# Optimization experiments

Hardware: AMD Instinct MI355X
Metric: run time of the kernel (lower is better)

## Reference

```python
import jax
import jax.numpy as jnp
import numpy as np

N_WIRES = 4          # hardcoded by QLayer encoder (rx on wires 0..3)
H = N_WIRES          # hidden_dim must equal n_qubits for the gating elementwise math
T, B, D, TAGS = 512, 2048, 8, 16  # original unbinds dim 0, so dim0 = time, dim1 = batch


def apply_rx(state, theta, wire):
    """Apply RX(theta) on `wire`. state: (B,2,2,2,2) complex64, theta: (B,)."""
    st = jnp.moveaxis(state, 1 + wire, -1)
    a, b = st[..., 0], st[..., 1]
    th = theta[:, None, None, None] * 0.5
    c = jnp.cos(th)
    s = -1j * jnp.sin(th)
    st = jnp.stack([c * a + s * b, s * a + c * b], axis=-1)
    return jnp.moveaxis(st, -1, 1 + wire)


def apply_cnot(state, ctrl, tgt):
    st = jnp.moveaxis(state, (1 + ctrl, 1 + tgt), (-2, -1))  # (...,2,2)
    st = st.at[..., 1, :].set(st[..., 1, ::-1])
    return jnp.moveaxis(st, (-2, -1), (1 + ctrl, 1 + tgt))


def qlayer(angles, thetas):
    """QuantumQLSTM.QLayer: RX data encoding, trainable RX, CNOT ring, PauliZ expvals.
    angles: (B, 4) data angles; thetas: (4,) trainable RX angles -> (B, 4) expvals."""
    bsz = angles.shape[0]
    state = jnp.zeros((bsz, 16), jnp.complex64).at[:, 0].set(1.0)
    state = state.reshape(bsz, 2, 2, 2, 2)
    for w in range(N_WIRES):
        state = apply_rx(state, angles[:, w], w)
    for w in range(N_WIRES):
        state = apply_rx(state, jnp.broadcast_to(thetas[w], (bsz,)), w)
    for w in range(N_WIRES):  # cnot(w, w+1), last wraps to 0
        state = apply_cnot(state, w, (w + 1) % N_WIRES)
    probs = state.real ** 2 + state.imag ** 2  # (B,2,2,2,2)
    exps = []
    for w in range(N_WIRES):
        sign = jnp.array([1.0, -1.0], jnp.float32).reshape(
            [1] + [2 if i == w else 1 for i in range(N_WIRES)])
        exps.append(jnp.sum(probs * sign, axis=(1, 2, 3, 4)))
    return jnp.stack(exps, axis=-1)  # (B, 4)


def lstm_forward(x, w_gates, b_gates, rx_theta):
    # Faithful to torch: inputs.unbind(dim=0) -> scan over axis 0; batch = x.shape[1].
    bsz = x.shape[1]
    h0 = jnp.zeros((bsz, H), x.dtype)
    c0 = jnp.zeros((bsz, H), x.dtype)

    def step(carry, xt):
        hx, cx = carry
        comb = jnp.concatenate([xt, hx], axis=-1)                    # (B, D+H)
        pre = jnp.einsum('bd,gkd->gbk', comb, w_gates) + b_gates[:, None, :]  # (4,B,4)
        f = jax.nn.sigmoid(qlayer(pre[0], rx_theta[0]))
        i = jax.nn.sigmoid(qlayer(pre[1], rx_theta[1]))
        g = jnp.tanh(qlayer(pre[2], rx_theta[2]))
        o = jax.nn.sigmoid(qlayer(pre[3], rx_theta[3]))
        cx = f * cx + i * g
        hx = o * jnp.tanh(cx)
        return (hx, cx), hx

    _, outs = jax.lax.scan(jax.checkpoint(step), (h0, c0), x)
    return outs  # (T, B, H)


def setup_inputs() -> dict:
    key = jax.random.key(0)
    ks = jax.random.split(key, 6)
    x = jax.random.normal(ks[0], (T, B, D), jnp.float32)
    w_gates = jax.random.normal(ks[1], (4, N_WIRES, D + H), jnp.float32) * 0.3
    b_gates = jnp.zeros((4, N_WIRES), jnp.float32)
    rx_theta = jax.random.uniform(ks[2], (4, N_WIRES), jnp.float32, 0.0, 2.0 * np.pi)
    w_tag = jax.random.normal(ks[3], (TAGS, H), jnp.float32) * 0.3
    b_tag = jnp.zeros((TAGS,), jnp.float32)
    return {"x": x, "w_gates": w_gates, "b_gates": b_gates,
            "rx_theta": rx_theta, "w_tag": w_tag, "b_tag": b_tag}


def reference(x, w_gates, b_gates, rx_theta, w_tag, b_tag):
    # encode(): SamplerQNN has input_params=[], so it cannot transform features;
    # features pass through to the QLSTM (see notes).
    outs = lstm_forward(x, w_gates, b_gates, rx_theta)   # (T, B, H)
    logits = outs @ w_tag.T + b_tag                      # (T, B, TAGS)
    return jax.nn.log_softmax(logits, axis=-1)
```

## Files before the change

kernel.cpp:

```cpp
#include <hip/hip_runtime.h>

#define TT   512
#define BB   2048
#define NTAG 16
#define CH   8
#define NCH  (TT / CH)
#define BBN  (BB * NTAG)

typedef float v2f __attribute__((ext_vector_type(2)));

#define DPP_XOR1  0xB1
#define DPP_XOR2  0x4E
#define DPP_XOR3  0x1B
#define DPP_ROR4  0x124
#define DPP_ROR8  0x128
#define DPP_ROR12 0x12C
#define DPP_BC0   0x00
#define DPP_BC1   0x55
#define DPP_BC2   0xAA
#define DPP_BC3   0xFF

template<int CTRL>
__device__ __forceinline__ float dppf(float v) {
    int r = __builtin_amdgcn_update_dpp(0, __builtin_bit_cast(int, v),
                                        CTRL, 0xF, 0xF, true);
    return __builtin_bit_cast(float, r);
}

#define PINV(x) asm volatile("" : "+v"(x))

__global__ __launch_bounds__(256, 1) void qlstm_fused(
    const float* __restrict__ x,
    const float* __restrict__ w_gates,
    const float* __restrict__ b_gates,
    const float* __restrict__ rx_theta,
    const float* __restrict__ w_tag,
    const float* __restrict__ b_tag,
    float* __restrict__ out)
{
    __shared__ float  accL[2][4][CH][64];
    __shared__ float  hrng[2][2][CH][64];
    __shared__ float4 xstg[2][2][64];

    const int tid = threadIdx.x;
    const int wv  = tid >> 6;
    const int l   = tid & 63;
    const int e   = l >> 4;

    const float IV  = 0.15915494309189535f;
    const float L2E = 1.44269504088896f;
    const float LN2 = 0.69314718056f;

    if (wv < 2) {
        const int s = wv;
        const int w = (l >> 2) & 3;
        const int G = l & 3;

        const float* wrow = w_gates + (G * 4 + w) * 12;
        float wh0 = wrow[8 + ((w + 0) & 3)] * IV;
        float wh1 = wrow[8 + ((w + 1) & 3)] * IV;
        float wh2 = wrow[8 + ((w + 2) & 3)] * IV;
        float wh3 = wrow[8 + ((w + 3) & 3)] * IV;

        const bool gt = (G == 2);
        float ab = gt ? 0.0f : 0.5f;
        float d0 = gt ? 0.999904f  : 0.25f;
        float d1 = gt ? -0.331065f : -0.0208333333f;
        float d2 = gt ? 0.120472f  : 0.00208333333f;
        float d3 = gt ? -0.027717f : -2.10813e-4f;

        float u0 = 0.999160f,  u1 = -0.325289f, u2 = 0.112257f;
        float u3 = -0.028766f, u4 = 0.0043665f, u5 = -0.00028186f;

        const bool w0 = (w == 0), w1 = (w == 1), w3 = (w == 3);

        PINV(wh0); PINV(wh1); PINV(wh2); PINV(wh3);
        PINV(ab);  PINV(d0);  PINV(d1);  PINV(d2);  PINV(d3);
        PINV(u0);  PINV(u1);  PINV(u2);  PINV(u3);  PINV(u4);  PINV(u5);

        const int atl = (l & 48) | ((l & 3) << 2) | ((l >> 2) & 3);

        float h = 0.f, c = 0.f;

        __syncthreads();

        float a[CH];
        {
            const float* ap0 = &accL[s][0][0][atl];
            #pragma unroll
            for (int i = 0; i < CH; ++i) a[i] = ap0[i * 64];
        }

        for (int cc = 0; cc < NCH; ++cc) {
            const float* np = &accL[s][(cc + 1) & 3][0][atl];
            float n[CH];
            #pragma unroll
            for (int i = 0; i < CH; ++i) n[i] = np[i * 64];

            float* hp = &hrng[s][cc & 1][0][l];

            #pragma unroll
            for (int i = 0; i < CH; ++i) {
                const float s1 = fmaf(h, wh0, a[i]);
                const float s2 = fmaf(dppf<DPP_ROR12>(h), wh1, s1);
                const float mm = dppf<DPP_ROR8>(h) * wh2;
                const float s3 = fmaf(dppf<DPP_ROR4>(h), wh3, mm);
                const float ang = s2 + s3;

                const float C = __builtin_amdgcn_cosf(ang);

                const float n1 = dppf<DPP_ROR12>(C);
                const float n2 = dppf<DPP_ROR8>(C);
                const float n3 = dppf<DPP_ROR4>(C);
                const float Bp = n2 * n3;
                const float pp = C * n1;
                const float F1  = w0 ? n1 : C;
                const float F1b = w3 ? pp : F1;
                const float F2  = w1 ? n3 : Bp;
                const float q   = F1b * F2;

                const float y  = q * q;
                const float y2 = y * y;
                const float tA = fmaf(y, d1, d0);
                const float tB = fmaf(y, d3, d2);
                const float P  = fmaf(y2, tB, tA);
                const float act = fmaf(q, P, ab);

                const float A2  = dppf<DPP_BC2>(act);
                const float A12 = dppf<DPP_BC1>(act) * A2;
                c = fmaf(dppf<DPP_BC0>(act), c, A12);

                const float voc = dppf<DPP_BC3>(act) * c;
                const float cy  = c * c;
                const float cy2 = cy * cy;
                const float t1  = fmaf(cy, u1, u0);
                const float t2  = fmaf(cy, u3, u2);
                const float t3  = fmaf(cy, u5, u4);
                const float t4  = fmaf(cy2, t3, t2);
                const float m1v = voc * t1;
                const float vc2 = voc * cy2;
                const float hr  = fmaf(vc2, t4, m1v);

                hp[i * 64] = hr;
                h = hr;
            }

            #pragma unroll
            for (int i = 0; i < CH; ++i) a[i] = n[i];

            __syncthreads();
        }
    } else {
        const int s  = wv - 2;
        const int b0 = blockIdx.x * 8 + s * 4;
        const int g  = (l >> 2) & 3;
        const int k  = l & 3;

        const float* wrow = w_gates + (g * 4 + k) * 12;
        const v2f wp0 = { wrow[0] * IV, wrow[1] * IV };
        const v2f wp1 = { wrow[2] * IV, wrow[3] * IV };
        const v2f wp2 = { wrow[4] * IV, wrow[5] * IV };
        const v2f wp3 = { wrow[6] * IV, wrow[7] * IV };
        const v2f bp  = { (b_gates[g * 4 + k] + rx_theta[g * 4 + k]) * IV, 0.0f };

        const int tag = g * 4 + k;
        const float wt0 = w_tag[tag * 4 + (k ^ 0)] * L2E;
        const float wt1 = w_tag[tag * 4 + (k ^ 1)] * L2E;
        const float wt2 = w_tag[tag * 4 + (k ^ 2)] * L2E;
        const float wt3 = w_tag[tag * 4 + (k ^ 3)] * L2E;
        const float bt  = b_tag[tag] * L2E;

        const int hsl = e * 16 + k * 4;
        float* outp = out + (size_t)b0 * NTAG + l;

        const float* xlane = x + (size_t)(l >> 3) * (BB * 8)
                               + (size_t)b0 * 8 + (l & 7) * 4;
        const size_t CHOFF = (size_t)CH * BB * 8;

        auto compute_acc = [&](int xbuf, int ring) {
            float* ap = &accL[s][ring][0][l];
            #pragma unroll
            for (int i = 0; i < CH; ++i) {
                const float4 xA = xstg[s][xbuf][i * 8 + 2 * e];
                const float4 xB = xstg[s][xbuf][i * 8 + 2 * e + 1];
                const v2f a01 = { xA.x, xA.y }, a23 = { xA.z, xA.w };
                const v2f a45 = { xB.x, xB.y }, a67 = { xB.z, xB.w };
                v2f acc = __builtin_elementwise_fma(a01, wp0, bp);
                acc = __builtin_elementwise_fma(a23, wp1, acc);
                acc = __builtin_elementwise_fma(a45, wp2, acc);
                acc = __builtin_elementwise_fma(a67, wp3, acc);
                ap[i * 64] = acc.x + acc.y;
            }
        };

        float4 reg = *(const float4*)(xlane);
        xstg[s][0][l] = reg;
        reg = *(const float4*)(xlane + CHOFF);
        xstg[s][1][l] = reg;
        compute_acc(0, 0);
        compute_acc(1, 1);
        reg = *(const float4*)(xlane + 2 * CHOFF);
        xstg[s][0][l] = reg;
        reg = *(const float4*)(xlane + 3 * CHOFF);
        __syncthreads();

        for (int cc = 0; cc < NCH; ++cc) {
            const int cur = cc & 1;

            if (cc + 2 < NCH) compute_acc(cur, (cc + 2) & 3);

            if (cc + 3 < NCH) {
                xstg[s][cur ^ 1][l] = reg;
                const int cn = (cc + 4 < NCH) ? cc + 4 : NCH - 1;
                reg = *(const float4*)(xlane + (size_t)cn * CHOFF);
            }

            if (cc > 0) {
                const float* hp = &hrng[s][cur ^ 1][0][hsl];
                #pragma unroll
                for (int i = 0; i < CH; ++i) {
                    const float hv = hp[i * 64];
                    const float q1 = dppf<DPP_XOR1>(hv);
                    const float q2 = dppf<DPP_XOR2>(hv);
                    const float q3 = dppf<DPP_XOR3>(hv);

                    const float lgq = fmaf(hv, wt0, fmaf(q1, wt1, fmaf(q2, wt2,
                                         fmaf(q3, wt3, bt))));
                    const float ex = __builtin_amdgcn_exp2f(lgq);
                    float sm = ex + dppf<DPP_XOR1>(ex);
                    sm = sm + dppf<DPP_XOR2>(sm);
                    sm = sm + dppf<DPP_ROR4>(sm);
                    sm = sm + dppf<DPP_ROR8>(sm);
                    const float l2s = __builtin_amdgcn_logf(sm);

                    *outp = (lgq - l2s) * LN2;
                    outp += BBN;
                }
            }
            __syncthreads();
        }

        {
            const float* hp = &hrng[s][1][0][hsl];
            #pragma unroll
            for (int i = 0; i < CH; ++i) {
                const float hv = hp[i * 64];
                const float q1 = dppf<DPP_XOR1>(hv);
                const float q2 = dppf<DPP_XOR2>(hv);
                const float q3 = dppf<DPP_XOR3>(hv);

                const float lgq = fmaf(hv, wt0, fmaf(q1, wt1, fmaf(q2, wt2,
                                     fmaf(q3, wt3, bt))));
                const float ex = __builtin_amdgcn_exp2f(lgq);
                float sm = ex + dppf<DPP_XOR1>(ex);
                sm = sm + dppf<DPP_XOR2>(sm);
                sm = sm + dppf<DPP_ROR4>(sm);
                sm = sm + dppf<DPP_ROR8>(sm);
                const float l2s = __builtin_amdgcn_logf(sm);

                *outp = (lgq - l2s) * LN2;
                outp += BBN;
            }
        }
    }
}

extern "C" void kernel_launch(void* const* d_in, const int* in_sizes, int n_in,
                              void* d_out, int out_size, void* d_ws, size_t ws_size,
                              hipStream_t stream) {
    const float* x        = (const float*)d_in[0];
    const float* w_gates  = (const float*)d_in[1];
    const float* b_gates  = (const float*)d_in[2];
    const float* rx_theta = (const float*)d_in[3];
    const float* w_tag    = (const float*)d_in[4];
    const float* b_tag    = (const float*)d_in[5];
    float* out = (float*)d_out;

    qlstm_fused<<<BB / 8, 256, 0, stream>>>(x, w_gates, b_gates, rx_theta,
                                            w_tag, b_tag, out);
}
```

Measured before the change: 136.7 us.

## Merge two recurrence waves into one using packed float2 math

Two recurrence wavefronts, each handling one sub-batch, become a single wavefront that carries both sub-batches as packed two-float vectors. Shared buffers are interleaved so the producer and consumer waves write and read their half of each pair, and the block shrinks from 256 to 192 threads. The aim is to use packed FMA/mul instructions to halve the issue count of the serial recurrence and free a wave slot. The cost is that DPP permutes and cos stay scalar, so they are doubled on one wave, and the serial chain per wave gets longer, which can lengthen the critical path.

```diff
diff --git a/kernel.cpp b/kernel.cpp
--- a/kernel.cpp
+++ b/kernel.cpp
@@ -27,9 +27,17 @@
     return __builtin_bit_cast(float, r);
 }
 
-#define PINV(x) asm volatile("" : "+v"(x))
-
-__global__ __launch_bounds__(256, 1) void qlstm_fused(
+template<int CTRL>
+__device__ __forceinline__ v2f dpp2(v2f v) {
+    v2f r;
+    r.x = dppf<CTRL>(v.x);
+    r.y = dppf<CTRL>(v.y);
+    return r;
+}
+
+#define FMA2(a, b, c) __builtin_elementwise_fma((a), (b), (c))
+
+__global__ __launch_bounds__(192, 1) void qlstm_fused(
     const float* __restrict__ x,
     const float* __restrict__ w_gates,
     const float* __restrict__ b_gates,
@@ -38,8 +46,8 @@
     const float* __restrict__ b_tag,
     float* __restrict__ out)
 {
-    __shared__ float  accL[2][4][CH][64];
-    __shared__ float  hrng[2][2][CH][64];
+    __shared__ v2f    accV[4][CH][64];
+    __shared__ v2f    hrnV[2][CH][64];
     __shared__ float4 xstg[2][2][64];
 
     const int tid = threadIdx.x;
@@ -51,95 +59,101 @@
     const float L2E = 1.44269504088896f;
     const float LN2 = 0.69314718056f;
 
-    if (wv < 2) {
-        const int s = wv;
+    if (wv == 0) {
         const int w = (l >> 2) & 3;
         const int G = l & 3;
 
         const float* wrow = w_gates + (G * 4 + w) * 12;
-        float wh0 = wrow[8 + ((w + 0) & 3)] * IV;
-        float wh1 = wrow[8 + ((w + 1) & 3)] * IV;
-        float wh2 = wrow[8 + ((w + 2) & 3)] * IV;
-        float wh3 = wrow[8 + ((w + 3) & 3)] * IV;
+        const float wh0 = wrow[8 + ((w + 0) & 3)] * IV;
+        const float wh1 = wrow[8 + ((w + 1) & 3)] * IV;
+        const float wh2 = wrow[8 + ((w + 2) & 3)] * IV;
+        const float wh3 = wrow[8 + ((w + 3) & 3)] * IV;
+        const v2f whp0 = { wh0, wh0 }, whp1 = { wh1, wh1 };
+        const v2f whp2 = { wh2, wh2 }, whp3 = { wh3, wh3 };
 
         const bool gt = (G == 2);
-        float ab = gt ? 0.0f : 0.5f;
-        float d0 = gt ? 0.999904f  : 0.25f;
-        float d1 = gt ? -0.331065f : -0.0208333333f;
-        float d2 = gt ? 0.120472f  : 0.00208333333f;
-        float d3 = gt ? -0.027717f : -2.10813e-4f;
-
-        float u0 = 0.999160f,  u1 = -0.325289f, u2 = 0.112257f;
-        float u3 = -0.028766f, u4 = 0.0043665f, u5 = -0.00028186f;
+        const float ab = gt ? 0.0f : 0.5f;
+        const float d0 = gt ? 0.999904f  : 0.25f;
+        const float d1 = gt ? -0.331065f : -0.0208333333f;
+        const float d2 = gt ? 0.120472f  : 0.00208333333f;
+        const float d3 = gt ? -0.027717f : -2.10813e-4f;
+        const v2f abp = { ab, ab };
+        const v2f d0p = { d0, d0 }, d1p = { d1, d1 };
+        const v2f d2p = { d2, d2 }, d3p = { d3, d3 };
+
+        const v2f u0p = { 0.999160f, 0.999160f };
+        const v2f u1p = { -0.325289f, -0.325289f };
+        const v2f u2p = { 0.112257f, 0.112257f };
+        const v2f u3p = { -0.028766f, -0.028766f };
+        const v2f u4p = { 0.0043665f, 0.0043665f };
+        const v2f u5p = { -0.00028186f, -0.00028186f };
 
         const bool w0 = (w == 0), w1 = (w == 1), w3 = (w == 3);
 
-        PINV(wh0); PINV(wh1); PINV(wh2); PINV(wh3);
-        PINV(ab);  PINV(d0);  PINV(d1);  PINV(d2);  PINV(d3);
-        PINV(u0);  PINV(u1);  PINV(u2);  PINV(u3);  PINV(u4);  PINV(u5);
-
         const int atl = (l & 48) | ((l & 3) << 2) | ((l >> 2) & 3);
 
-        float h = 0.f, c = 0.f;
+        v2f h = { 0.f, 0.f }, c = { 0.f, 0.f };
 
         __syncthreads();
 
-        float a[CH];
+        v2f a[CH];
         {
-            const float* ap0 = &accL[s][0][0][atl];
+            const v2f* ap0 = &accV[0][0][atl];
             #pragma unroll
             for (int i = 0; i < CH; ++i) a[i] = ap0[i * 64];
         }
 
         for (int cc = 0; cc < NCH; ++cc) {
-            const float* np = &accL[s][(cc + 1) & 3][0][atl];
-            float n[CH];
+            const v2f* np = &accV[(cc + 1) & 3][0][atl];
+            v2f n[CH];
             #pragma unroll
             for (int i = 0; i < CH; ++i) n[i] = np[i * 64];
 
-            float* hp = &hrng[s][cc & 1][0][l];
+            v2f* hp = &hrnV[cc & 1][0][l];
 
             #pragma unroll
             for (int i = 0; i < CH; ++i) {
-                const float s1 = fmaf(h, wh0, a[i]);
-                const float s2 = fmaf(dppf<DPP_ROR12>(h), wh1, s1);
-                const float mm = dppf<DPP_ROR8>(h) * wh2;
-                const float s3 = fmaf(dppf<DPP_ROR4>(h), wh3, mm);
-                const float ang = s2 + s3;
-
-                const float C = __builtin_amdgcn_cosf(ang);
-
-                const float n1 = dppf<DPP_ROR12>(C);
-                const float n2 = dppf<DPP_ROR8>(C);
-                const float n3 = dppf<DPP_ROR4>(C);
-                const float Bp = n2 * n3;
-                const float pp = C * n1;
-                const float F1  = w0 ? n1 : C;
-                const float F1b = w3 ? pp : F1;
-                const float F2  = w1 ? n3 : Bp;
-                const float q   = F1b * F2;
-
-                const float y  = q * q;
-                const float y2 = y * y;
-                const float tA = fmaf(y, d1, d0);
-                const float tB = fmaf(y, d3, d2);
-                const float P  = fmaf(y2, tB, tA);
-                const float act = fmaf(q, P, ab);
-
-                const float A2  = dppf<DPP_BC2>(act);
-                const float A12 = dppf<DPP_BC1>(act) * A2;
-                c = fmaf(dppf<DPP_BC0>(act), c, A12);
-
-                const float voc = dppf<DPP_BC3>(act) * c;
-                const float cy  = c * c;
-                const float cy2 = cy * cy;
-                const float t1  = fmaf(cy, u1, u0);
-                const float t2  = fmaf(cy, u3, u2);
-                const float t3  = fmaf(cy, u5, u4);
-                const float t4  = fmaf(cy2, t3, t2);
-                const float m1v = voc * t1;
-                const float vc2 = voc * cy2;
-                const float hr  = fmaf(vc2, t4, m1v);
+                const v2f s1 = FMA2(h, whp0, a[i]);
+                const v2f s2 = FMA2(dpp2<DPP_ROR12>(h), whp1, s1);
+                const v2f mm = dpp2<DPP_ROR8>(h) * whp2;
+                const v2f s3 = FMA2(dpp2<DPP_ROR4>(h), whp3, mm);
+                const v2f ang = s2 + s3;
+
+                v2f C;
+                C.x = __builtin_amdgcn_cosf(ang.x);
+                C.y = __builtin_amdgcn_cosf(ang.y);
+
+                const v2f n1 = dpp2<DPP_ROR12>(C);
+                const v2f n2 = dpp2<DPP_ROR8>(C);
+                const v2f n3 = dpp2<DPP_ROR4>(C);
+                const v2f Bp = n2 * n3;
+                const v2f pp = C * n1;
+                const v2f F1  = w0 ? n1 : C;
+                const v2f F1b = w3 ? pp : F1;
+                const v2f F2  = w1 ? n3 : Bp;
+                const v2f q   = F1b * F2;
+
+                const v2f y  = q * q;
+                const v2f y2 = y * y;
+                const v2f tA = FMA2(y, d1p, d0p);
+                const v2f tB = FMA2(y, d3p, d2p);
+                const v2f P  = FMA2(y2, tB, tA);
+                const v2f act = FMA2(q, P, abp);
+
+                const v2f A2  = dpp2<DPP_BC2>(act);
+                const v2f A12 = dpp2<DPP_BC1>(act) * A2;
+                c = FMA2(dpp2<DPP_BC0>(act), c, A12);
+
+                const v2f voc = dpp2<DPP_BC3>(act) * c;
+                const v2f cy  = c * c;
+                const v2f cy2 = cy * cy;
+                const v2f t1  = FMA2(cy, u1p, u0p);
+                const v2f t2  = FMA2(cy, u3p, u2p);
+                const v2f t3  = FMA2(cy, u5p, u4p);
+                const v2f t4  = FMA2(cy2, t3, t2);
+                const v2f m1v = voc * t1;
+                const v2f vc2 = voc * cy2;
+                const v2f hr  = FMA2(vc2, t4, m1v);
 
                 hp[i * 64] = hr;
                 h = hr;
@@ -151,7 +165,7 @@
             __syncthreads();
         }
     } else {
-        const int s  = wv - 2;
+        const int s  = wv - 1;
         const int b0 = blockIdx.x * 8 + s * 4;
         const int g  = (l >> 2) & 3;
         const int k  = l & 3;
@@ -178,18 +192,18 @@
         const size_t CHOFF = (size_t)CH * BB * 8;
 
         auto compute_acc = [&](int xbuf, int ring) {
-            float* ap = &accL[s][ring][0][l];
+            float* ap = (float*)&accV[ring][0][l];
             #pragma unroll
             for (int i = 0; i < CH; ++i) {
                 const float4 xA = xstg[s][xbuf][i * 8 + 2 * e];
                 const float4 xB = xstg[s][xbuf][i * 8 + 2 * e + 1];
                 const v2f a01 = { xA.x, xA.y }, a23 = { xA.z, xA.w };
                 const v2f a45 = { xB.x, xB.y }, a67 = { xB.z, xB.w };
-                v2f acc = __builtin_elementwise_fma(a01, wp0, bp);
-                acc = __builtin_elementwise_fma(a23, wp1, acc);
-                acc = __builtin_elementwise_fma(a45, wp2, acc);
-                acc = __builtin_elementwise_fma(a67, wp3, acc);
-                ap[i * 64] = acc.x + acc.y;
+                v2f acc = FMA2(a01, wp0, bp);
+                acc = FMA2(a23, wp1, acc);
+                acc = FMA2(a45, wp2, acc);
+                acc = FMA2(a67, wp3, acc);
+                ap[i * 128 + s] = acc.x + acc.y;
             }
         };
 
@@ -216,10 +230,10 @@
             }
 
             if (cc > 0) {
-                const float* hp = &hrng[s][cur ^ 1][0][hsl];
+                const float* hpf = (const float*)&hrnV[cur ^ 1][0][hsl];
                 #pragma unroll
                 for (int i = 0; i < CH; ++i) {
-                    const float hv = hp[i * 64];
+                    const float hv = hpf[i * 128 + s];
                     const float q1 = dppf<DPP_XOR1>(hv);
                     const float q2 = dppf<DPP_XOR2>(hv);
                     const float q3 = dppf<DPP_XOR3>(hv);
@@ -241,10 +255,10 @@
         }
 
         {
-            const float* hp = &hrng[s][1][0][hsl];
+            const float* hpf = (const float*)&hrnV[1][0][hsl];
             #pragma unroll
             for (int i = 0; i < CH; ++i) {
-                const float hv = hp[i * 64];
+                const float hv = hpf[i * 128 + s];
                 const float q1 = dppf<DPP_XOR1>(hv);
                 const float q2 = dppf<DPP_XOR2>(hv);
                 const float q3 = dppf<DPP_XOR3>(hv);
@@ -276,6 +290,6 @@
     const float* b_tag    = (const float*)d_in[5];
     float* out = (float*)d_out;
 
-    qlstm_fused<<<BB / 8, 256, 0, stream>>>(x, w_gates, b_gates, rx_theta,
+    qlstm_fused<<<BB / 8, 192, 0, stream>>>(x, w_gates, b_gates, rx_theta,
                                             w_tag, b_tag, out);
 }
```

After: 156.5 us. +14.5%, slower.
